# Performance work log

Measured on AMD Instinct MI355X. Metric: run time of the kernel, lower is better.

## Reference

```python
import jax, jax.numpy as jnp
import numpy as np

EPS = 1e-6
TOP_K = 2


def setup_inputs() -> dict:
    key = jax.random.key(0)
    k0, k1, k2, k3, k4 = jax.random.split(key, 5)
    B, S, H, I, E = 1, 2048, 1024, 3584, 8
    return {
        "hidden_states": jax.random.normal(k0, (B, S, H), jnp.float32),
        "rms_weight": jnp.ones((H,), jnp.float32),
        "gate_w": jax.random.normal(k1, (E, H), jnp.float32) * (H ** -0.5),
        "w1": jax.random.normal(k2, (E, I, H), jnp.float32) * (H ** -0.5),
        "w2": jax.random.normal(k3, (E, H, I), jnp.float32) * (I ** -0.5),
        "w3": jax.random.normal(k4, (E, I, H), jnp.float32) * (H ** -0.5),
    }


def reference(hidden_states, rms_weight, gate_w, w1, w2, w3):
    B, S, H = hidden_states.shape
    E = gate_w.shape[0]
    # RMSNorm (fp32 internally, matches _RMSNorm)
    x = hidden_states.astype(jnp.float32)
    var = jnp.mean(x * x, axis=-1, keepdims=True)
    h = rms_weight * (x * jax.lax.rsqrt(var + EPS))  # [B,S,H]
    # Router: softmax over experts, top-k, renormalize
    logits = jnp.einsum('bsh,eh->bse', h, gate_w)
    scores = jax.nn.softmax(logits.astype(jnp.float32), axis=-1)
    top_w, top_i = jax.lax.top_k(scores, TOP_K)        # [B,S,K]
    top_w = top_w / jnp.sum(top_w, axis=-1, keepdims=True)
    top_w = top_w.astype(h.dtype)
    # Per-token combine weight for every expert: cw[t,e]
    hf = h.reshape(-1, H)                               # [T,H]
    oh = jax.nn.one_hot(top_i.reshape(-1, TOP_K), E, dtype=h.dtype)  # [T,K,E]
    cw = jnp.einsum('tke,tk->te', oh, top_w.reshape(-1, TOP_K))       # [T,E]
    # SwiGLU expert MLPs, batched over experts (dense dispatch; weights zero out unrouted tokens)
    a = jnp.einsum('th,eih->eti', hf, w1)               # [E,T,I]
    g = jnp.einsum('th,eih->eti', hf, w3)               # [E,T,I]
    eo = jnp.einsum('eti,ehi->eth', jax.nn.silu(a) * g, w2)  # [E,T,H]
    out = jnp.einsum('eth,te->th', eo, cw)              # [T,H]
    return hidden_states + out.reshape(B, S, H)
```

## Files before the change

### kernel.cpp

```cpp
#include <hip/hip_runtime.h>
#include <hip/hip_bf16.h>
#include <stdint.h>

#define T_TOK 2048
#define HDIM  1024
#define IDIM  3584
#define NEXP  8
#define NROWS 4096
#define WELEM 29360128
#define NJOBS 40
#define CVTB  512

typedef __attribute__((ext_vector_type(8))) short bf16x8;
typedef __attribute__((ext_vector_type(4))) float f32x4;

typedef __attribute__((address_space(3))) unsigned lds_u32;
typedef const __attribute__((address_space(1))) unsigned glb_u32;

#define MFMA16 __builtin_amdgcn_mfma_f32_16x16x32_bf16

__device__ __forceinline__ unsigned short f2bf(float f){
  union { float f; unsigned u; } v; v.f = f;
  unsigned r = v.u + 0x7FFFu + ((v.u >> 16) & 1u);
  return (unsigned short)(r >> 16);
}
__device__ __forceinline__ unsigned cvt2(float a, float b){
  __hip_bfloat162 h = __float22bfloat162_rn(float2{a, b});
  return *reinterpret_cast<unsigned*>(&h);
}

__global__ __launch_bounds__(256) void k_rms_router(
    const float* __restrict__ x, const float* __restrict__ rmsw,
    const float* __restrict__ gw, unsigned short* __restrict__ h_bf,
    int* __restrict__ topk_i, float* __restrict__ topk_w, int* __restrict__ count,
    const float4* __restrict__ w1s, const float4* __restrict__ w3s,
    uint2* __restrict__ w1d, uint2* __restrict__ w3d)
{
  const int t = blockIdx.x, tid = threadIdx.x;
  const int lane = tid & 63, wid = tid >> 6;
  float4 x4 = reinterpret_cast<const float4*>(x)[t*256 + tid];
  float ss = x4.x*x4.x + x4.y*x4.y + x4.z*x4.z + x4.w*x4.w;
  #pragma unroll
  for (int o = 32; o >= 1; o >>= 1) ss += __shfl_xor(ss, o);
  __shared__ float sred[4];
  __shared__ float slog[32];
  if (lane == 0) sred[wid] = ss;
  __syncthreads();
  float inv = rsqrtf((sred[0]+sred[1]+sred[2]+sred[3]) * (1.0f/HDIM) + 1e-6f);
  float4 w4 = reinterpret_cast<const float4*>(rmsw)[tid];
  float h0 = x4.x*inv*w4.x, h1 = x4.y*inv*w4.y, h2 = x4.z*inv*w4.z, h3 = x4.w*inv*w4.w;
  ushort4 hb; hb.x = f2bf(h0); hb.y = f2bf(h1); hb.z = f2bf(h2); hb.w = f2bf(h3);
  reinterpret_cast<ushort4*>(h_bf)[t*256 + tid] = hb;
  #pragma unroll
  for (int e = 0; e < NEXP; e++){
    float4 g4 = reinterpret_cast<const float4*>(gw)[e*256 + tid];
    float v = h0*g4.x + h1*g4.y + h2*g4.z + h3*g4.w;
    #pragma unroll
    for (int o = 32; o >= 1; o >>= 1) v += __shfl_xor(v, o);
    if (lane == 0) slog[e*4 + wid] = v;
  }
  __syncthreads();
  if (tid == 0){
    float lg[NEXP];
    #pragma unroll
    for (int e = 0; e < NEXP; e++) lg[e] = slog[e*4]+slog[e*4+1]+slog[e*4+2]+slog[e*4+3];
    int i0 = 0;
    for (int e = 1; e < NEXP; e++) if (lg[e] > lg[i0]) i0 = e;
    int i1 = -1;
    for (int e = 0; e < NEXP; e++){ if (e == i0) continue; if (i1 < 0 || lg[e] > lg[i1]) i1 = e; }
    float m  = fmaxf(lg[i0], lg[i1]);
    float e0 = expf(lg[i0]-m), e1 = expf(lg[i1]-m);
    float s  = e0 + e1;
    topk_i[t*2] = i0; topk_i[t*2+1] = i1;
    topk_w[t*2] = e0/s; topk_w[t*2+1] = e1/s;
    atomicAdd(&count[i0], 1); atomicAdd(&count[i1], 1);
  }
  const int stride = 2048*256;
  for (int i = t*256 + tid; i < WELEM/4; i += stride){
    float4 a = w1s[i];
    w1d[i] = make_uint2(cvt2(a.x, a.y), cvt2(a.z, a.w));
    float4 b = w3s[i];
    w3d[i] = make_uint2(cvt2(b.x, b.y), cvt2(b.z, b.w));
  }
}

__global__ void k_scan(const int* __restrict__ count, int* __restrict__ offset,
                       int* __restrict__ jobs){
  if (threadIdx.x == 0){
    int o = 0, L = 0;
    for (int e = 0; e < NEXP; e++){
      offset[e] = o;
      int nrt = (count[e] + 127) >> 7;
      for (int r = 0; r < nrt && L < NJOBS; r++) jobs[L++] = (e << 8) | r;
      o += count[e];
    }
    for (; L < NJOBS; L++) jobs[L] = -1;
  }
}

__global__ __launch_bounds__(256) void k_scatter(
    const int* __restrict__ topk_i, const float* __restrict__ topk_w,
    const int* __restrict__ offset, int* __restrict__ cursor,
    int* __restrict__ token_of_row, float* __restrict__ wrow, int* __restrict__ slot_of)
{
  int t = blockIdx.x*256 + threadIdx.x;
  if (t >= T_TOK) return;
  #pragma unroll
  for (int k = 0; k < 2; k++){
    int e = topk_i[t*2+k];
    int pos = atomicAdd(&cursor[e], 1);
    int row = offset[e] + pos;
    token_of_row[row] = t;
    wrow[row] = topk_w[t*2+k];
    slot_of[t*2+k] = row;
  }
}

__global__ __launch_bounds__(256) void k_cvt(
    const float4* __restrict__ src, uint2* __restrict__ dst, int n4)
{
  int stride = gridDim.x * blockDim.x;
  for (int i = blockIdx.x*blockDim.x + threadIdx.x; i < n4; i += stride){
    float4 v = src[i];
    dst[i] = make_uint2(cvt2(v.x, v.y), cvt2(v.z, v.w));
  }
}

__global__ __launch_bounds__(256, 3) void k_mlp_in(
    const unsigned short* __restrict__ h_bf, const unsigned short* __restrict__ w1bf,
    const unsigned short* __restrict__ w3bf, const int* __restrict__ token_of_row,
    const int* __restrict__ count, const int* __restrict__ offset,
    const int* __restrict__ jobs, unsigned short* __restrict__ act,
    const float4* __restrict__ w2s, uint2* __restrict__ w2d)
{
  const int d = blockIdx.x;
  const int tid = threadIdx.x;
  if (d >= NJOBS*56){
    if (w2d){
      int i0 = (d - NJOBS*56)*256 + tid;
      for (int i = i0; i < WELEM/4; i += CVTB*256){
        float4 v = w2s[i];
        w2d[i] = make_uint2(cvt2(v.x, v.y), cvt2(v.z, v.w));
      }
    }
    return;
  }
  const int p = d % 56;
  const int t = d / 56;
  const int job = jobs[t];
  if (job < 0) return;
  const int e = job >> 8, rt = job & 255;
  const int cnt = count[e];
  const int off = offset[e], row0 = off + rt*128, rend = off + cnt;
  const int col0 = p * 64;
  const int lane = tid & 63, wid = tid >> 6;
  const int wave_r = wid >> 1, wave_c = wid & 1;

  __shared__ __align__(16) char sA [16384];
  __shared__ __align__(16) char sB1[8192];
  __shared__ __align__(16) char sB2[8192];

  const int srow = tid >> 3;
  const int sg   = (tid & 7) ^ (srow & 7);

  const unsigned short* aptr[4];
  #pragma unroll
  for (int j = 0; j < 4; j++){
    int tok = token_of_row[min(row0 + srow + 32*j, NROWS-1)];
    aptr[j] = h_bf + (size_t)tok*HDIM + sg*8;
  }
  const unsigned short* b1ptr[2];
  const unsigned short* b3ptr[2];
  #pragma unroll
  for (int j = 0; j < 2; j++){
    int col = col0 + srow + 32*j;
    b1ptr[j] = w1bf + (size_t)(e*IDIM + col)*HDIM + sg*8;
    b3ptr[j] = w3bf + (size_t)(e*IDIM + col)*HDIM + sg*8;
  }

  #define ISSUE(kk) {                                                                \
    _Pragma("unroll")                                                                \
    for (int j = 0; j < 4; j++)                                                      \
      __builtin_amdgcn_global_load_lds((glb_u32*)(const void*)(aptr[j] + (kk)*64),   \
          (lds_u32*)(void*)(sA + j*4096 + tid*16), 16, 0, 0);                        \
    _Pragma("unroll")                                                                \
    for (int j = 0; j < 2; j++){                                                     \
      __builtin_amdgcn_global_load_lds((glb_u32*)(const void*)(b1ptr[j] + (kk)*64),  \
          (lds_u32*)(void*)(sB1 + j*4096 + tid*16), 16, 0, 0);                       \
      __builtin_amdgcn_global_load_lds((glb_u32*)(const void*)(b3ptr[j] + (kk)*64),  \
          (lds_u32*)(void*)(sB2 + j*4096 + tid*16), 16, 0, 0);                       \
    } }

  f32x4 acc1[4][2], acc3[4][2];
  #pragma unroll
  for (int m = 0; m < 4; m++)
    #pragma unroll
    for (int n = 0; n < 2; n++){
      acc1[m][n] = (f32x4){0.f,0.f,0.f,0.f};
      acc3[m][n] = (f32x4){0.f,0.f,0.f,0.f};
    }

  for (int kk = 0; kk < HDIM/64; kk++){
    ISSUE(kk);
    __syncthreads();
    #pragma unroll
    for (int ki = 0; ki < 2; ki++){
      bf16x8 af[4];
      #pragma unroll
      for (int m = 0; m < 4; m++){
        int row = wave_r*64 + m*16 + (lane & 15);
        int slot = ki*4 + (lane >> 4);
        af[m] = *reinterpret_cast<const bf16x8*>(sA + row*128 + ((slot ^ (row&7))<<4));
      }
      #pragma unroll
      for (int n = 0; n < 2; n++){
        int col = wave_c*32 + n*16 + (lane & 15);
        int slot = ki*4 + (lane >> 4);
        bf16x8 b1 = *reinterpret_cast<const bf16x8*>(sB1 + col*128 + ((slot ^ (col&7))<<4));
        bf16x8 b2 = *reinterpret_cast<const bf16x8*>(sB2 + col*128 + ((slot ^ (col&7))<<4));
        #pragma unroll
        for (int m = 0; m < 4; m++){
          acc1[m][n] = MFMA16(af[m], b1, acc1[m][n], 0,0,0);
          acc3[m][n] = MFMA16(af[m], b2, acc3[m][n], 0,0,0);
        }
      }
    }
    __syncthreads();
  }

  const int lcol = lane & 15, lrow4 = (lane >> 4) * 4;
  #pragma unroll
  for (int m = 0; m < 4; m++){
    #pragma unroll
    for (int n = 0; n < 2; n++){
      int gcol = col0 + wave_c*32 + n*16 + lcol;
      #pragma unroll
      for (int r = 0; r < 4; r++){
        int grow = row0 + wave_r*64 + m*16 + lrow4 + r;
        if (grow < rend){
          float a = acc1[m][n][r], g = acc3[m][n][r];
          float sig = 1.0f / (1.0f + __expf(-a));
          act[(size_t)grow*IDIM + gcol] = f2bf(a * sig * g);
        }
      }
    }
  }
  #undef ISSUE
}

__global__ __launch_bounds__(256, 3) void k_mlp_out(
    const unsigned short* __restrict__ act, const unsigned short* __restrict__ w2bf,
    const float* __restrict__ wrow, const int* __restrict__ count,
    const int* __restrict__ offset, const int* __restrict__ jobs,
    float* __restrict__ eo)
{
  const int d = blockIdx.x;
  const int p = d & 15;
  const int t = d >> 4;
  const int job = jobs[t];
  if (job < 0) return;
  const int e = job >> 8, rt = job & 255;
  const int cnt = count[e];
  const int off = offset[e], row0 = off + rt*128, rend = off + cnt;
  const int col0 = p * 64;
  const int tid = threadIdx.x, lane = tid & 63, wid = tid >> 6;
  const int wave_r = wid >> 1, wave_c = wid & 1;

  __shared__ __align__(16) char sA[32768];
  __shared__ __align__(16) char sB[16384];

  const int sr16 = tid >> 4;
  const int sg   = (tid & 15) ^ sr16;

  const unsigned short* aptr[8];
  #pragma unroll
  for (int j = 0; j < 8; j++){
    int r = min(row0 + j*16 + sr16, NROWS-1);
    aptr[j] = act + (size_t)r*IDIM + sg*8;
  }
  const unsigned short* bptr[4];
  #pragma unroll
  for (int j = 0; j < 4; j++){
    int col = col0 + j*16 + sr16;
    bptr[j] = w2bf + (size_t)(e*HDIM + col)*IDIM + sg*8;
  }

  #define ISSUE(kk) {                                                                \
    _Pragma("unroll")                                                                \
    for (int j = 0; j < 8; j++)                                                      \
      __builtin_amdgcn_global_load_lds((glb_u32*)(const void*)(aptr[j] + (kk)*128),  \
          (lds_u32*)(void*)(sA + j*4096 + tid*16), 16, 0, 0);                        \
    _Pragma("unroll")                                                                \
    for (int j = 0; j < 4; j++)                                                      \
      __builtin_amdgcn_global_load_lds((glb_u32*)(const void*)(bptr[j] + (kk)*128),  \
          (lds_u32*)(void*)(sB + j*4096 + tid*16), 16, 0, 0); }

  f32x4 acc[4][2];
  #pragma unroll
  for (int m = 0; m < 4; m++)
    #pragma unroll
    for (int n = 0; n < 2; n++) acc[m][n] = (f32x4){0.f,0.f,0.f,0.f};

  for (int kk = 0; kk < IDIM/128; kk++){
    ISSUE(kk);
    __syncthreads();
    #pragma unroll
    for (int ki = 0; ki < 4; ki++){
      bf16x8 af[4];
      #pragma unroll
      for (int m = 0; m < 4; m++){
        int row = wave_r*64 + m*16 + (lane & 15);
        int slot = ki*4 + (lane >> 4);
        af[m] = *reinterpret_cast<const bf16x8*>(sA + row*256 + ((slot ^ (row&15))<<4));
      }
      #pragma unroll
      for (int n = 0; n < 2; n++){
        int col = wave_c*32 + n*16 + (lane & 15);
        int slot = ki*4 + (lane >> 4);
        bf16x8 fb = *reinterpret_cast<const bf16x8*>(sB + col*256 + ((slot ^ (col&15))<<4));
        #pragma unroll
        for (int m = 0; m < 4; m++)
          acc[m][n] = MFMA16(af[m], fb, acc[m][n], 0,0,0);
      }
    }
    __syncthreads();
  }

  const int lcol = lane & 15, lrow4 = (lane >> 4) * 4;
  #pragma unroll
  for (int m = 0; m < 4; m++){
    #pragma unroll
    for (int n = 0; n < 2; n++){
      int gcol = col0 + wave_c*32 + n*16 + lcol;
      #pragma unroll
      for (int r = 0; r < 4; r++){
        int grow = row0 + wave_r*64 + m*16 + lrow4 + r;
        if (grow < rend){
          eo[(size_t)grow*HDIM + gcol] = acc[m][n][r] * wrow[grow];
        }
      }
    }
  }
  #undef ISSUE
}

__global__ __launch_bounds__(256) void k_combine(
    const float* __restrict__ x, const float* __restrict__ eo,
    const int* __restrict__ slot_of, float* __restrict__ out)
{
  const int t = blockIdx.x, tid = threadIdx.x;
  const int s0 = slot_of[t*2], s1 = slot_of[t*2+1];
  float4 xv = reinterpret_cast<const float4*>(x)[t*256 + tid];
  float4 a  = reinterpret_cast<const float4*>(eo)[s0*256 + tid];
  float4 b  = reinterpret_cast<const float4*>(eo)[s1*256 + tid];
  float4 ov;
  ov.x = xv.x + a.x + b.x;
  ov.y = xv.y + a.y + b.y;
  ov.z = xv.z + a.z + b.z;
  ov.w = xv.w + a.w + b.w;
  reinterpret_cast<float4*>(out)[t*256 + tid] = ov;
}

extern "C" void kernel_launch(void* const* d_in, const int* in_sizes, int n_in,
                              void* d_out, int out_size, void* d_ws, size_t ws_size,
                              hipStream_t stream)
{
  const float* x    = (const float*)d_in[0];
  const float* rmsw = (const float*)d_in[1];
  const float* gw   = (const float*)d_in[2];
  const float* w1   = (const float*)d_in[3];
  const float* w2   = (const float*)d_in[4];
  const float* w3   = (const float*)d_in[5];
  float* out = (float*)d_out;

  char* ws = (char*)d_ws;
  size_t o = 0;
  auto alloc = [&](size_t bytes) -> void* {
    void* p = ws + o;
    o += (bytes + 255) & ~(size_t)255;
    return p;
  };
  unsigned short* h_bf   = (unsigned short*)alloc((size_t)T_TOK*HDIM*2);
  int*   topk_i          = (int*)  alloc(T_TOK*2*4);
  float* topk_w          = (float*)alloc(T_TOK*2*4);
  int*   counters        = (int*)  alloc(64*4);
  int*   jobs            = (int*)  alloc(NJOBS*4);
  int*   token_of_row    = (int*)  alloc(NROWS*4);
  float* wrow            = (float*)alloc(NROWS*4);
  int*   slot_of         = (int*)  alloc(T_TOK*2*4);
  unsigned short* act    = (unsigned short*)alloc((size_t)NROWS*IDIM*2);
  float* eo              = (float*)alloc((size_t)NROWS*HDIM*4);
  int* count  = counters;
  int* cursor = counters + 8;
  int* offset = counters + 16;

  bool have3 = (ws_size >= o + (size_t)3*WELEM*2);
  unsigned short* w1bf = (unsigned short*)(ws + o);
  unsigned short* w3bf = w1bf + WELEM;
  unsigned short* w2bf = have3 ? (w3bf + WELEM) : w1bf;

  hipMemsetAsync(counters, 0, 64*4, stream);
  k_rms_router<<<T_TOK, 256, 0, stream>>>(x, rmsw, gw, h_bf, topk_i, topk_w, count,
                                          (const float4*)w1, (const float4*)w3,
                                          (uint2*)w1bf, (uint2*)w3bf);
  k_scan<<<1, 64, 0, stream>>>(count, offset, jobs);
  k_scatter<<<(T_TOK+255)/256, 256, 0, stream>>>(topk_i, topk_w, offset, cursor,
                                                 token_of_row, wrow, slot_of);
  k_mlp_in<<<NJOBS*56 + (have3 ? CVTB : 0), 256, 0, stream>>>(
      h_bf, w1bf, w3bf, token_of_row, count, offset, jobs, act,
      (const float4*)w2, have3 ? (uint2*)w2bf : (uint2*)nullptr);
  if (!have3)
    k_cvt<<<2048, 256, 0, stream>>>((const float4*)w2, (uint2*)w2bf, WELEM/4);
  k_mlp_out<<<NJOBS*16, 256, 0, stream>>>(act, w2bf, wrow, count, offset, jobs, eo);
  k_combine<<<T_TOK, 256, 0, stream>>>(x, eo, slot_of, out);
}
```

Measured before the change: 298.6 us.

## Fuse fp32-to-bf16 conversion of w1/w3 into the expert up-projection GEMM

Drops the separate pass in the router kernel that converted all of w1 and w3 to bf16 in workspace. The up-projection GEMM now loads fp32 weight tiles directly into enlarged LDS buffers with a new XOR swizzle and packs them to bf16 just before the MFMA. This removes a full read-write-read round trip of two large weight tensors. In exchange, the GEMM reads twice the bytes per weight tile, uses more LDS (which may reduce occupancy at 3 blocks per CU), and does conversion work inside the inner loop, repeated for each row tile of the same expert.

```diff
diff --git a/kernel.cpp b/kernel.cpp
--- a/kernel.cpp
+++ b/kernel.cpp
@@ -28,13 +28,19 @@
   __hip_bfloat162 h = __float22bfloat162_rn(float2{a, b});
   return *reinterpret_cast<unsigned*>(&h);
 }
+__device__ __forceinline__ bf16x8 pack8(float4 lo, float4 hi){
+  union { __hip_bfloat162 b2[4]; bf16x8 v; } u;
+  u.b2[0] = __float22bfloat162_rn(float2{lo.x, lo.y});
+  u.b2[1] = __float22bfloat162_rn(float2{lo.z, lo.w});
+  u.b2[2] = __float22bfloat162_rn(float2{hi.x, hi.y});
+  u.b2[3] = __float22bfloat162_rn(float2{hi.z, hi.w});
+  return u.v;
+}
 
 __global__ __launch_bounds__(256) void k_rms_router(
     const float* __restrict__ x, const float* __restrict__ rmsw,
     const float* __restrict__ gw, unsigned short* __restrict__ h_bf,
-    int* __restrict__ topk_i, float* __restrict__ topk_w, int* __restrict__ count,
-    const float4* __restrict__ w1s, const float4* __restrict__ w3s,
-    uint2* __restrict__ w1d, uint2* __restrict__ w3d)
+    int* __restrict__ topk_i, float* __restrict__ topk_w, int* __restrict__ count)
 {
   const int t = blockIdx.x, tid = threadIdx.x;
   const int lane = tid & 63, wid = tid >> 6;
@@ -75,13 +81,6 @@
     topk_w[t*2] = e0/s; topk_w[t*2+1] = e1/s;
     atomicAdd(&count[i0], 1); atomicAdd(&count[i1], 1);
   }
-  const int stride = 2048*256;
-  for (int i = t*256 + tid; i < WELEM/4; i += stride){
-    float4 a = w1s[i];
-    w1d[i] = make_uint2(cvt2(a.x, a.y), cvt2(a.z, a.w));
-    float4 b = w3s[i];
-    w3d[i] = make_uint2(cvt2(b.x, b.y), cvt2(b.z, b.w));
-  }
 }
 
 __global__ void k_scan(const int* __restrict__ count, int* __restrict__ offset,
@@ -127,8 +126,8 @@
 }
 
 __global__ __launch_bounds__(256, 3) void k_mlp_in(
-    const unsigned short* __restrict__ h_bf, const unsigned short* __restrict__ w1bf,
-    const unsigned short* __restrict__ w3bf, const int* __restrict__ token_of_row,
+    const unsigned short* __restrict__ h_bf, const float* __restrict__ w1,
+    const float* __restrict__ w3, const int* __restrict__ token_of_row,
     const int* __restrict__ count, const int* __restrict__ offset,
     const int* __restrict__ jobs, unsigned short* __restrict__ act,
     const float4* __restrict__ w2s, uint2* __restrict__ w2d)
@@ -157,26 +156,20 @@
   const int wave_r = wid >> 1, wave_c = wid & 1;
 
   __shared__ __align__(16) char sA [16384];
-  __shared__ __align__(16) char sB1[8192];
-  __shared__ __align__(16) char sB2[8192];
+  __shared__ __align__(16) char sB1[16384];
+  __shared__ __align__(16) char sB3[16384];
 
   const int srow = tid >> 3;
   const int sg   = (tid & 7) ^ (srow & 7);
-
   const unsigned short* aptr[4];
   #pragma unroll
   for (int j = 0; j < 4; j++){
     int tok = token_of_row[min(row0 + srow + 32*j, NROWS-1)];
     aptr[j] = h_bf + (size_t)tok*HDIM + sg*8;
   }
-  const unsigned short* b1ptr[2];
-  const unsigned short* b3ptr[2];
-  #pragma unroll
-  for (int j = 0; j < 2; j++){
-    int col = col0 + srow + 32*j;
-    b1ptr[j] = w1bf + (size_t)(e*IDIM + col)*HDIM + sg*8;
-    b3ptr[j] = w3bf + (size_t)(e*IDIM + col)*HDIM + sg*8;
-  }
+  const int bl = (tid & 15) ^ ((tid >> 4) & 15);
+  const float* b1base = w1 + ((size_t)e*IDIM + col0 + (tid >> 4))*HDIM + bl*4;
+  const float* b3base = w3 + ((size_t)e*IDIM + col0 + (tid >> 4))*HDIM + bl*4;
 
   #define ISSUE(kk) {                                                                \
     _Pragma("unroll")                                                                \
@@ -184,11 +177,13 @@
       __builtin_amdgcn_global_load_lds((glb_u32*)(const void*)(aptr[j] + (kk)*64),   \
           (lds_u32*)(void*)(sA + j*4096 + tid*16), 16, 0, 0);                        \
     _Pragma("unroll")                                                                \
-    for (int j = 0; j < 2; j++){                                                     \
-      __builtin_amdgcn_global_load_lds((glb_u32*)(const void*)(b1ptr[j] + (kk)*64),  \
+    for (int j = 0; j < 4; j++){                                                     \
+      __builtin_amdgcn_global_load_lds(                                              \
+          (glb_u32*)(const void*)(b1base + (size_t)j*16*HDIM + (kk)*64),             \
           (lds_u32*)(void*)(sB1 + j*4096 + tid*16), 16, 0, 0);                       \
-      __builtin_amdgcn_global_load_lds((glb_u32*)(const void*)(b3ptr[j] + (kk)*64),  \
-          (lds_u32*)(void*)(sB2 + j*4096 + tid*16), 16, 0, 0);                       \
+      __builtin_amdgcn_global_load_lds(                                              \
+          (glb_u32*)(const void*)(b3base + (size_t)j*16*HDIM + (kk)*64),             \
+          (lds_u32*)(void*)(sB3 + j*4096 + tid*16), 16, 0, 0);                       \
     } }
 
   f32x4 acc1[4][2], acc3[4][2];
@@ -214,14 +209,20 @@
       }
       #pragma unroll
       for (int n = 0; n < 2; n++){
-        int col = wave_c*32 + n*16 + (lane & 15);
-        int slot = ki*4 + (lane >> 4);
-        bf16x8 b1 = *reinterpret_cast<const bf16x8*>(sB1 + col*128 + ((slot ^ (col&7))<<4));
-        bf16x8 b2 = *reinterpret_cast<const bf16x8*>(sB2 + col*128 + ((slot ^ (col&7))<<4));
+        int c  = wave_c*32 + n*16 + (lane & 15);
+        int l0 = ki*8 + (lane >> 4)*2;
+        int p0 = (l0     ^ (c & 15)) << 4;
+        int p1 = ((l0+1) ^ (c & 15)) << 4;
+        float4 lo1 = *reinterpret_cast<const float4*>(sB1 + c*256 + p0);
+        float4 hi1 = *reinterpret_cast<const float4*>(sB1 + c*256 + p1);
+        float4 lo3 = *reinterpret_cast<const float4*>(sB3 + c*256 + p0);
+        float4 hi3 = *reinterpret_cast<const float4*>(sB3 + c*256 + p1);
+        bf16x8 b1 = pack8(lo1, hi1);
+        bf16x8 b3 = pack8(lo3, hi3);
         #pragma unroll
         for (int m = 0; m < 4; m++){
           acc1[m][n] = MFMA16(af[m], b1, acc1[m][n], 0,0,0);
-          acc3[m][n] = MFMA16(af[m], b2, acc3[m][n], 0,0,0);
+          acc3[m][n] = MFMA16(af[m], b3, acc3[m][n], 0,0,0);
         }
       }
     }
@@ -394,22 +395,18 @@
   int* cursor = counters + 8;
   int* offset = counters + 16;
 
-  bool have3 = (ws_size >= o + (size_t)3*WELEM*2);
-  unsigned short* w1bf = (unsigned short*)(ws + o);
-  unsigned short* w3bf = w1bf + WELEM;
-  unsigned short* w2bf = have3 ? (w3bf + WELEM) : w1bf;
+  bool havew2 = (ws_size >= o + (size_t)WELEM*2);
+  unsigned short* w2bf = (unsigned short*)(ws + o);
 
   hipMemsetAsync(counters, 0, 64*4, stream);
-  k_rms_router<<<T_TOK, 256, 0, stream>>>(x, rmsw, gw, h_bf, topk_i, topk_w, count,
-                                          (const float4*)w1, (const float4*)w3,
-                                          (uint2*)w1bf, (uint2*)w3bf);
+  k_rms_router<<<T_TOK, 256, 0, stream>>>(x, rmsw, gw, h_bf, topk_i, topk_w, count);
   k_scan<<<1, 64, 0, stream>>>(count, offset, jobs);
   k_scatter<<<(T_TOK+255)/256, 256, 0, stream>>>(topk_i, topk_w, offset, cursor,
                                                  token_of_row, wrow, slot_of);
-  k_mlp_in<<<NJOBS*56 + (have3 ? CVTB : 0), 256, 0, stream>>>(
-      h_bf, w1bf, w3bf, token_of_row, count, offset, jobs, act,
-      (const float4*)w2, have3 ? (uint2*)w2bf : (uint2*)nullptr);
-  if (!have3)
+  k_mlp_in<<<NJOBS*56 + (havew2 ? CVTB : 0), 256, 0, stream>>>(
+      h_bf, w1, w3, token_of_row, count, offset, jobs, act,
+      (const float4*)w2, havew2 ? (uint2*)w2bf : (uint2*)nullptr);
+  if (!havew2)
     k_cvt<<<2048, 256, 0, stream>>>((const float4*)w2, (uint2*)w2bf, WELEM/4);
   k_mlp_out<<<NJOBS*16, 256, 0, stream>>>(act, w2bf, wrow, count, offset, jobs, eo);
   k_combine<<<T_TOK, 256, 0, stream>>>(x, eo, slot_of, out);
```

Result: no change. 297.7 us (median of 2 runs) (-0.3%).
